# Kernel tuning notes

Measured on AMD Instinct MI355X. Metric: run time of the kernel, lower is better.

## Reference

```python
import jax, jax.numpy as jnp
import numpy as np

# qshift_a: Kingsbury 10-tap Q-shift filters (sum(h0a) = sqrt(2)).
_H0A = np.array([0.0351638365171441, 0.0, -0.0883294244510729,
                 0.233890320607236, 0.760272369066126, 0.587518297723561,
                 0.0, -0.114301837144249, 0.0, 0.0], dtype=np.float64)
_H0B = _H0A[::-1].copy()
_ALT = (-1.0) ** np.arange(10)
_H1A = _H0B * _ALT            # highpass tree a
_H1B = _H1A[::-1].copy()
# synthesis filters (g0a = h0b, g0b = h0a, g1a = h1b, g1b = h1a)
G0A = _H0B.astype(np.float32)
G0B = _H0A.astype(np.float32)
G1A = _H1B.astype(np.float32)
G1B = _H1A.astype(np.float32)


def _reflect(x, minx, maxx):
    # dtcwt symmetric-extension index reflection (static, numpy)
    x = np.asarray(x, dtype=np.float64)
    rng = maxx - minx
    rng2 = 2.0 * rng
    mod = np.fmod(x - minx, rng2)
    normed = np.where(mod < 0, mod + rng2, mod)
    out = np.where(normed >= rng, rng2 - normed, normed) + minx
    return out.astype(np.int64)


def _colifilt(X, ha, hb):
    # X: (B, C, r, c) -> (B, C, 2r, c). ha, hb are 1-D numpy filters (static).
    m = ha.shape[0]
    m2 = m // 2
    assert m2 % 2 == 1, 'implemented for 10/14/18-tap qshift (m/2 odd)'
    b, ch, r, c = X.shape
    r2 = r // 2
    xe = _reflect(np.arange(-m2, r + m2), -0.5, r - 0.5)   # static indices
    t = np.arange(2, r + m - 1, 2)
    if float(np.sum(ha * hb)) > 0:
        ta, tb = t, t - 1
    else:
        ta, tb = t - 1, t
    Xa = X[:, :, xe[ta], :]   # (B, C, r/2 + m/2 - 1, c)
    Xb = X[:, :, xe[tb], :]
    hao, hae = ha[0::2], ha[1::2]
    hbo, hbe = hb[0::2], hb[1::2]

    def vconv(Z, h):
        # valid convolution along dim 2 (true conv: filter flipped)
        hf = h[::-1]
        out = Z[:, :, 0:r2, :] * float(hf[0])
        for k in range(1, m2):
            out = out + Z[:, :, k:k + r2, :] * float(hf[k])
        return out

    y = jnp.stack([vconv(Xb, hao), vconv(Xa, hbo),
                   vconv(Xb, hae), vconv(Xa, hbe)], axis=3)  # (B,C,r/2,4,c)
    return y.reshape(b, ch, 2 * r, c)


def _rowifilt(X, ha, hb):
    return jnp.swapaxes(_colifilt(jnp.swapaxes(X, 2, 3), ha, hb), 2, 3)


def _c2q(wr, wi):
    # complex pair of subbands -> real quad image. wr, wi: (B, C, 2, H, W) -> (B, C, 2H, 2W)
    w1r, w2r = wr[:, :, 0], wr[:, :, 1]
    w1i, w2i = wi[:, :, 0], wi[:, :, 1]
    x1 = w1r + w2r
    x2 = w1i + w2i
    x3 = w1i - w2i
    x4 = w2r - w1r
    b, c, h, w = x1.shape
    top = jnp.stack([x1, x2], axis=-1).reshape(b, c, h, 2 * w)
    bot = jnp.stack([x3, x4], axis=-1).reshape(b, c, h, 2 * w)
    y = jnp.stack([top, bot], axis=-2).reshape(b, c, 2 * h, 2 * w)
    return y * np.float32(1.0 / np.sqrt(2.0))


def setup_inputs() -> dict:
    key = jax.random.key(0)
    k1, k2, k3 = jax.random.split(key, 3)
    B, C, H, W = 8, 64, 128, 128
    Yl = jax.random.normal(k1, (B, C, H, W), dtype=jnp.float32)
    Yhr = jax.random.normal(k2, (B, C, 6, H // 2, W // 2), dtype=jnp.float32)
    Yhi = jax.random.normal(k3, (B, C, 6, H // 2, W // 2), dtype=jnp.float32)
    return {"Yl": Yl, "Yhr": Yhr, "Yhi": Yhi}


def reference(Yl, Yhr, Yhi):
    lh = _c2q(Yhr[:, :, 0:6:5], Yhi[:, :, 0:6:5])
    hl = _c2q(Yhr[:, :, 2:4:1], Yhi[:, :, 2:4:1])
    hh = _c2q(Yhr[:, :, 1:5:3], Yhi[:, :, 1:5:3])
    y1 = _rowifilt(Yl, G0B, G0A) + _rowifilt(hl, G1B, G1A)
    y2 = _rowifilt(lh, G0B, G0A) + _rowifilt(hh, G1B, G1A)
    return _colifilt(y1, G0B, G0A) + _colifilt(y2, G1B, G1A)
```

## Files before the change

kernel.cpp:

```cpp
#include <hip/hip_runtime.h>
#include <hip/hip_bf16.h>

#define NTHREADS 256

__device__ __forceinline__ int reflect128(int p) {
    p = (p < 0) ? (-p - 1) : p;
    p = (p >= 128) ? (255 - p) : p;
    return p;
}

__constant__ int   cs0[4] = {2, 1, 1, 0};
__constant__ int   cs1[4] = {1, 2, 0, 1};
__constant__ float cc0[4][3] = {
    { 0.760272369066126f, -0.0883294244510729f,  0.0351638365171441f},
    { 0.233890320607236f,  0.587518297723561f,  -0.114301837144249f},
    {-0.114301837144249f,  0.587518297723561f,   0.233890320607236f},
    { 0.0351638365171441f, -0.0883294244510729f, 0.760272369066126f}};
__constant__ float cc1[4][3] = {
    { 0.233890320607236f,  0.587518297723561f,  -0.114301837144249f},
    {-0.760272369066126f,  0.0883294244510729f, -0.0351638365171441f},
    {-0.0351638365171441f, 0.0883294244510729f, -0.760272369066126f},
    {-0.114301837144249f,  0.587518297723561f,   0.233890320607236f}};

__global__ __launch_bounds__(NTHREADS, 5)
void dtcwt_inv_kernel(const float* __restrict__ Yl,
                      const float* __restrict__ Yhr,
                      const float* __restrict__ Yhi,
                      float* __restrict__ out)
{
    const int tid   = threadIdx.x;
    const int ct    = blockIdx.x;
    const int rt    = blockIdx.y;
    const int plane = blockIdx.z;

    const int OR0 = rt * 64, OC0 = ct * 64;
    const int i0r = OR0 >> 2, i0c = OC0 >> 2;
    const int yrb = 2 * i0r - 4;
    const int icb = 2 * i0c - 4;

    const float* yl = Yl + (size_t)plane * (128 * 128);
    const float* hr = Yhr + (size_t)plane * 6 * 4096;
    const float* hi = Yhi + (size_t)plane * 6 * 4096;

    __shared__ float sLh[40][40];
    __shared__ float sHl[40][40];
    __shared__ float sHh[40][40];
    __shared__ __hip_bfloat16 sY1[40][64];
    __shared__ __hip_bfloat16 sY2[40][64];

    const float RS2 = 0.70710678118654752440f;

    for (int e = tid; e < 400; e += NTHREADS) {
        const int t2 = e / 20;
        const int u2 = e - t2 * 20;
        const int ar = i0r - 2 + t2;
        const int ac = i0c - 2 + u2;
        const int oobr = (ar < 0) | (ar >= 64);
        const int oobc = (ac < 0) | (ac >= 64);
        const int r2 = oobr ? ((ar < 0) ? (-ar - 1) : (127 - ar)) : ar;
        const int c2 = oobc ? ((ac < 0) ? (-ac - 1) : (127 - ac)) : ac;
        const int off = r2 * 64 + c2;
        const float ar0 = hr[off], ar1 = hr[4096 + off], ar2 = hr[2 * 4096 + off];
        const float ar3 = hr[3 * 4096 + off], ar4 = hr[4 * 4096 + off], ar5 = hr[5 * 4096 + off];
        const float ai0 = hi[off], ai1 = hi[4096 + off], ai2 = hi[2 * 4096 + off];
        const float ai3 = hi[3 * 4096 + off], ai4 = hi[4 * 4096 + off], ai5 = hi[5 * 4096 + off];
#pragma unroll
        for (int dt = 0; dt < 2; ++dt) {
#pragma unroll
            for (int du = 0; du < 2; ++du) {
                const int p = dt ^ oobr;
                const int q = du ^ oobc;
                const float sA = (p & q) ? -RS2 : RS2;
                const float sB = (p & (q ^ 1)) ? -RS2 : RS2;
                float b0, b5, b2v, b3, b1, b4;
                if (p == q) { b0 = ar0; b5 = ar5; b2v = ar2; b3 = ar3; b1 = ar1; b4 = ar4; }
                else        { b0 = ai0; b5 = ai5; b2v = ai2; b3 = ai3; b1 = ai1; b4 = ai4; }
                const int t = 2 * t2 + dt, u = 2 * u2 + du;
                sLh[t][u] = sA * b0 + sB * b5;
                sHl[t][u] = sA * b2v + sB * b3;
                sHh[t][u] = sA * b1 + sB * b4;
            }
        }
    }
    __syncthreads();

    const int c  = tid & 63;
    const int jc = c & 3;
    const int q2 = c >> 2;
    const float a0 = cc0[jc][0], a1 = cc0[jc][1], a2 = cc0[jc][2];
    const float b0w = cc1[jc][0], b1w = cc1[jc][1], b2w = cc1[jc][2];
    const int ub0 = 2 * q2 + (jc & 1) + 2 * cs0[jc];
    const int ub1 = 2 * q2 + ((jc & 1) ^ 1) + 2 * cs1[jc];
    const int ic0 = reflect128(icb + ub0);
    const int ic1 = reflect128(icb + ub0 + 2);
    const int ic2 = reflect128(icb + ub0 + 4);

    for (int t = tid >> 6; t < 40; t += 4) {
        const int ry = reflect128(yrb + t);
        const float* yrow = yl + ry * 128;
        float acc1 = yrow[ic0] * a0 + yrow[ic1] * a1 + yrow[ic2] * a2
                   + sHl[t][ub1] * b0w + sHl[t][ub1 + 2] * b1w + sHl[t][ub1 + 4] * b2w;
        float acc2 = sLh[t][ub0] * a0 + sLh[t][ub0 + 2] * a1 + sLh[t][ub0 + 4] * a2
                   + sHh[t][ub1] * b0w + sHh[t][ub1 + 2] * b1w + sHh[t][ub1 + 4] * b2w;
        sY1[t][c] = __float2bfloat16(acc1);
        sY2[t][c] = __float2bfloat16(acc2);
    }
    __syncthreads();

    const int j  = tid >> 6;
    const int p0 = j & 1, p1 = p0 ^ 1;
    const int r0 = p0 + 2 * cs0[j];
    const int r1 = p1 + 2 * cs1[j];
    const float d0 = cc0[j][0], d1 = cc0[j][1], d2 = cc0[j][2];
    const float e0 = cc1[j][0], e1 = cc1[j][1], e2 = cc1[j][2];

    float* op = out + ((size_t)plane * 256 + OR0 + j) * 256 + OC0 + c;
#pragma unroll
    for (int m = 0; m < 16; ++m) {
        float acc = __bfloat162float(sY1[2 * m + r0][c]) * d0
                  + __bfloat162float(sY1[2 * m + r0 + 2][c]) * d1
                  + __bfloat162float(sY1[2 * m + r0 + 4][c]) * d2
                  + __bfloat162float(sY2[2 * m + r1][c]) * e0
                  + __bfloat162float(sY2[2 * m + r1 + 2][c]) * e1
                  + __bfloat162float(sY2[2 * m + r1 + 4][c]) * e2;
        op[(size_t)m * 1024] = acc;
    }
}

extern "C" void kernel_launch(void* const* d_in, const int* in_sizes, int n_in,
                              void* d_out, int out_size, void* d_ws, size_t ws_size,
                              hipStream_t stream) {
    const float* Yl  = (const float*)d_in[0];
    const float* Yhr = (const float*)d_in[1];
    const float* Yhi = (const float*)d_in[2];
    float* out = (float*)d_out;

    const int planes = in_sizes[0] / (128 * 128);
    dim3 grid(4, 4, planes);
    dtcwt_inv_kernel<<<grid, NTHREADS, 0, stream>>>(Yl, Yhr, Yhi, out);
}
```

Baseline: 273.2 us.

## Keep row-filtered intermediates in registers and stage Yl tile in LDS

Result: faster. 262.0 us (-4.1%).

```diff
diff --git a/kernel.cpp b/kernel.cpp
--- a/kernel.cpp
+++ b/kernel.cpp
@@ -1,5 +1,4 @@
 #include <hip/hip_runtime.h>
-#include <hip/hip_bf16.h>
 
 #define NTHREADS 256
 
@@ -22,7 +21,7 @@
     {-0.0351638365171441f, 0.0883294244510729f, -0.760272369066126f},
     {-0.114301837144249f,  0.587518297723561f,   0.233890320607236f}};
 
-__global__ __launch_bounds__(NTHREADS, 5)
+__global__ __launch_bounds__(NTHREADS, 6)
 void dtcwt_inv_kernel(const float* __restrict__ Yl,
                       const float* __restrict__ Yhr,
                       const float* __restrict__ Yhi,
@@ -45,10 +44,17 @@
     __shared__ float sLh[40][40];
     __shared__ float sHl[40][40];
     __shared__ float sHh[40][40];
-    __shared__ __hip_bfloat16 sY1[40][64];
-    __shared__ __hip_bfloat16 sY2[40][64];
+    __shared__ float sYl[40][40];
 
     const float RS2 = 0.70710678118654752440f;
+
+    for (int e = tid; e < 1600; e += NTHREADS) {
+        const int t = e / 40;
+        const int u = e - t * 40;
+        const int r2 = reflect128(yrb + t);
+        const int c2 = reflect128(icb + u);
+        sYl[t][u] = yl[r2 * 128 + c2];
+    }
 
     for (int e = tid; e < 400; e += NTHREADS) {
         const int t2 = e / 20;
@@ -85,45 +91,41 @@
     __syncthreads();
 
     const int c  = tid & 63;
+    const int g  = tid >> 6;
     const int jc = c & 3;
     const int q2 = c >> 2;
-    const float a0 = cc0[jc][0], a1 = cc0[jc][1], a2 = cc0[jc][2];
+    const float a0  = cc0[jc][0], a1  = cc0[jc][1], a2  = cc0[jc][2];
     const float b0w = cc1[jc][0], b1w = cc1[jc][1], b2w = cc1[jc][2];
     const int ub0 = 2 * q2 + (jc & 1) + 2 * cs0[jc];
     const int ub1 = 2 * q2 + ((jc & 1) ^ 1) + 2 * cs1[jc];
-    const int ic0 = reflect128(icb + ub0);
-    const int ic1 = reflect128(icb + ub0 + 2);
-    const int ic2 = reflect128(icb + ub0 + 4);
 
-    for (int t = tid >> 6; t < 40; t += 4) {
-        const int ry = reflect128(yrb + t);
-        const float* yrow = yl + ry * 128;
-        float acc1 = yrow[ic0] * a0 + yrow[ic1] * a1 + yrow[ic2] * a2
-                   + sHl[t][ub1] * b0w + sHl[t][ub1 + 2] * b1w + sHl[t][ub1 + 4] * b2w;
-        float acc2 = sLh[t][ub0] * a0 + sLh[t][ub0 + 2] * a1 + sLh[t][ub0 + 4] * a2
-                   + sHh[t][ub1] * b0w + sHh[t][ub1 + 2] * b1w + sHh[t][ub1 + 4] * b2w;
-        sY1[t][c] = __float2bfloat16(acc1);
-        sY2[t][c] = __float2bfloat16(acc2);
+    const int tb = 8 * g;
+    float y1v[14], y2v[14];
+#pragma unroll
+    for (int k = 0; k < 14; ++k) {
+        const int t = tb + 1 + k;
+        y1v[k] = sYl[t][ub0] * a0  + sYl[t][ub0 + 2] * a1  + sYl[t][ub0 + 4] * a2
+               + sHl[t][ub1] * b0w + sHl[t][ub1 + 2] * b1w + sHl[t][ub1 + 4] * b2w;
+        y2v[k] = sLh[t][ub0] * a0  + sLh[t][ub0 + 2] * a1  + sLh[t][ub0 + 4] * a2
+               + sHh[t][ub1] * b0w + sHh[t][ub1 + 2] * b1w + sHh[t][ub1 + 4] * b2w;
     }
-    __syncthreads();
 
-    const int j  = tid >> 6;
-    const int p0 = j & 1, p1 = p0 ^ 1;
-    const int r0 = p0 + 2 * cs0[j];
-    const int r1 = p1 + 2 * cs1[j];
-    const float d0 = cc0[j][0], d1 = cc0[j][1], d2 = cc0[j][2];
-    const float e0 = cc1[j][0], e1 = cc1[j][1], e2 = cc1[j][2];
-
-    float* op = out + ((size_t)plane * 256 + OR0 + j) * 256 + OC0 + c;
+    float* op = out + ((size_t)plane * 256 + OR0 + 16 * g) * 256 + OC0 + c;
 #pragma unroll
-    for (int m = 0; m < 16; ++m) {
-        float acc = __bfloat162float(sY1[2 * m + r0][c]) * d0
-                  + __bfloat162float(sY1[2 * m + r0 + 2][c]) * d1
-                  + __bfloat162float(sY1[2 * m + r0 + 4][c]) * d2
-                  + __bfloat162float(sY2[2 * m + r1][c]) * e0
-                  + __bfloat162float(sY2[2 * m + r1 + 2][c]) * e1
-                  + __bfloat162float(sY2[2 * m + r1 + 4][c]) * e2;
-        op[(size_t)m * 1024] = acc;
+    for (int j = 0; j < 4; ++j) {
+        const int p0 = j & 1, p1 = p0 ^ 1;
+        const int r0 = p0 + 2 * cs0[j];
+        const int r1 = p1 + 2 * cs1[j];
+        const float d0 = cc0[j][0], d1 = cc0[j][1], d2 = cc0[j][2];
+        const float e0 = cc1[j][0], e1 = cc1[j][1], e2 = cc1[j][2];
+#pragma unroll
+        for (int mm = 0; mm < 4; ++mm) {
+            const int k0 = 2 * mm + r0 - 1;
+            const int k1 = 2 * mm + r1 - 1;
+            const float acc = y1v[k0] * d0 + y1v[k0 + 2] * d1 + y1v[k0 + 4] * d2
+                            + y2v[k1] * e0 + y2v[k1 + 2] * e1 + y2v[k1 + 4] * e2;
+            op[(size_t)(4 * mm + j) * 256] = acc;
+        }
     }
 }
 
```
